# Optimization experiments

Measured on AMD Instinct MI355X. Metric: run time of the kernel, lower is better.

## Reference

```python
import jax, jax.numpy as jnp
import numpy as np

N = 50000       # nodes
E = 800000      # edges (before self-loops)
F_IN = 128      # per-head input features (nfeat * t_size, t_size=1)
NHID = 128
NHEADS = 4
NCLASS = 64
NEG_SLOPE = 0.2   # GATConv leakyrelu negative_slope
ALPHA = 0.2       # outer LeakyReLU(alpha)


def setup_inputs():
    key = jax.random.key(0)
    ks = jax.random.split(key, 10)
    type_emb = jax.random.normal(ks[0], (NHEADS, N, F_IN), jnp.float32)
    edge = jax.random.randint(ks[1], (2, E), 0, N, dtype=jnp.int32)
    W = jax.random.normal(ks[2], (NHEADS, F_IN, NHID), jnp.float32) / np.sqrt(F_IN).astype(np.float32)
    att_src = jax.random.normal(ks[3], (NHEADS, NHID), jnp.float32) * 0.1
    att_dst = jax.random.normal(ks[4], (NHEADS, NHID), jnp.float32) * 0.1
    bias = jnp.zeros((NHEADS, NHID), jnp.float32)
    W_out = jax.random.normal(ks[5], (NHID * NHEADS, NCLASS), jnp.float32) / np.sqrt(NHID * NHEADS).astype(np.float32)
    att_src_out = jax.random.normal(ks[6], (NCLASS,), jnp.float32) * 0.1
    att_dst_out = jax.random.normal(ks[7], (NCLASS,), jnp.float32) * 0.1
    bias_out = jnp.zeros((NCLASS,), jnp.float32)
    return {"type_emb": type_emb, "edge": edge, "W": W, "att_src": att_src,
            "att_dst": att_dst, "bias": bias, "W_out": W_out,
            "att_src_out": att_src_out, "att_dst_out": att_dst_out,
            "bias_out": bias_out}


def _gat_conv(x, src, dst, W, a_src, a_dst, b):
    """PyG GATConv, heads=1, with self-loops already in (src, dst)."""
    xs = x @ W                                      # [N, H]
    e = jax.nn.leaky_relu((xs @ a_src)[src] + (xs @ a_dst)[dst], NEG_SLOPE)  # [E']
    # segment softmax over destination nodes (every node has a self-loop -> no empty segment)
    m = jax.ops.segment_max(e, dst, num_segments=N)
    ex = jnp.exp(e - m[dst])
    denom = jax.ops.segment_sum(ex, dst, num_segments=N)
    alpha = ex / denom[dst]                          # [E']
    out = jax.ops.segment_sum(alpha[:, None] * xs[src], dst, num_segments=N)  # [N, H]
    return out + b


def reference(type_emb, edge, W, att_src, att_dst, bias, W_out,
              att_src_out, att_dst_out, bias_out):
    loop = jnp.arange(N, dtype=edge.dtype)
    src = jnp.concatenate([edge[0], loop])
    dst = jnp.concatenate([edge[1], loop])
    # per-head GraphAttentionLayer: GATConv -> LeakyReLU(alpha) (dropout inactive)
    heads = [jax.nn.leaky_relu(
                 _gat_conv(type_emb[i], src, dst, W[i], att_src[i], att_dst[i], bias[i]),
                 ALPHA)
             for i in range(NHEADS)]
    x = jnp.concatenate(heads, axis=1)               # [N, NHID*NHEADS]
    y = jax.nn.leaky_relu(
            _gat_conv(x, src, dst, W_out, att_src_out, att_dst_out, bias_out),
            ALPHA)
    return jnp.tanh(y)                               # [N, NCLASS]
```

## Files before the change

kernel.cpp:

```cpp
#include <hip/hip_runtime.h>
#include <cmath>

#define NN 50000
#define EE 800000
#define ETOT (EE + NN)
#define NSCAN ((NN + 1023) / 1024)
#define SROWS 50048

typedef __bf16 v8bf __attribute__((ext_vector_type(8)));
typedef float f32x4 __attribute__((ext_vector_type(4)));
typedef float f32x2 __attribute__((ext_vector_type(2)));

__device__ __forceinline__ float lrelu(float x){ return x > 0.0f ? x : 0.2f * x; }
__device__ __forceinline__ unsigned short f2bf_rne(float x){
  unsigned int u = __float_as_uint(x);
  u += 0x7fffu + ((u >> 16) & 1u);
  return (unsigned short)(u >> 16);
}
__device__ __forceinline__ float bf2f(unsigned short b){
  return __uint_as_float(((unsigned int)b) << 16);
}
__device__ __forceinline__ void fma8p(f32x2* acc, float w, uint4 u){
  f32x2 w2 = {w, w};
  f32x2 a0, a1, a2, a3;
  a0[0] = __uint_as_float(u.x << 16); a0[1] = __uint_as_float(u.x & 0xffff0000u);
  a1[0] = __uint_as_float(u.y << 16); a1[1] = __uint_as_float(u.y & 0xffff0000u);
  a2[0] = __uint_as_float(u.z << 16); a2[1] = __uint_as_float(u.z & 0xffff0000u);
  a3[0] = __uint_as_float(u.w << 16); a3[1] = __uint_as_float(u.w & 0xffff0000u);
  acc[0] += w2 * a0;
  acc[1] += w2 * a1;
  acc[2] += w2 * a2;
  acc[3] += w2 * a3;
}

__global__ void k_hist(const int* __restrict__ dst, int* __restrict__ cnt){
  int i = blockIdx.x * 256 + threadIdx.x;
  if (i >= ETOT) return;
  int d = (i < EE) ? dst[i] : (i - EE);
  atomicAdd(&cnt[d], 1);
}

__global__ void k_scan1(const int* __restrict__ cnt, int* __restrict__ part){
  __shared__ int sm[256];
  int b = blockIdx.x, t = threadIdx.x;
  int base = b * 1024 + t * 4;
  int s = 0;
  #pragma unroll
  for (int j = 0; j < 4; j++) if (base + j < NN) s += cnt[base + j];
  sm[t] = s; __syncthreads();
  for (int off = 128; off; off >>= 1){
    if (t < off) sm[t] += sm[t + off];
    __syncthreads();
  }
  if (t == 0) part[b] = sm[0];
}

__global__ void k_scan2(const int* __restrict__ part, int* __restrict__ part2){
  if (threadIdx.x == 0 && blockIdx.x == 0){
    int run = 0;
    for (int i = 0; i < NSCAN; i++){ part2[i] = run; run += part[i]; }
  }
}

__global__ void k_scan3(const int* __restrict__ cnt, const int* __restrict__ part2,
                        int* __restrict__ rowptr){
  __shared__ int sm[256];
  int b = blockIdx.x, t = threadIdx.x;
  int base = b * 1024 + t * 4;
  int v[4]; int s = 0;
  #pragma unroll
  for (int j = 0; j < 4; j++){ v[j] = (base + j < NN) ? cnt[base + j] : 0; s += v[j]; }
  sm[t] = s; __syncthreads();
  for (int off = 1; off < 256; off <<= 1){
    int x = (t >= off) ? sm[t - off] : 0;
    __syncthreads();
    sm[t] += x;
    __syncthreads();
  }
  int run = part2[b] + sm[t] - s;
  #pragma unroll
  for (int j = 0; j < 4; j++){
    if (base + j < NN){ rowptr[base + j] = run; run += v[j]; }
  }
  if (b == 0 && t == 0) rowptr[NN] = ETOT;
}

__global__ void k_scatter(const int* __restrict__ src, const int* __restrict__ dst,
                          const int* __restrict__ rowptr, int* __restrict__ fill,
                          int* __restrict__ csr){
  int i = blockIdx.x * 256 + threadIdx.x;
  if (i >= ETOT) return;
  int s, d;
  if (i < EE){ s = src[i]; d = dst[i]; } else { s = d = i - EE; }
  int pos = rowptr[d] + atomicAdd(&fill[d], 1);
  csr[pos] = s;
}

__global__ void k_convB(const float* __restrict__ B, unsigned short* __restrict__ bh,
                        unsigned short* __restrict__ bl, int K, int N, int total){
  int i = blockIdx.x * 256 + threadIdx.x;
  if (i >= total) return;
  int per = K * N;
  int h = i / per, rem = i - h * per;
  int k = rem / N, n = rem - k * N;
  float x = B[i];
  unsigned short hb = f2bf_rne(x);
  unsigned short lb = f2bf_rne(x - bf2f(hb));
  size_t o = (size_t)h * per + ((size_t)(k >> 3) * N + n) * 8 + (k & 7);
  bh[o] = hb; bl[o] = lb;
}

template<int BN, int OSTR>
__global__ __launch_bounds__(256) void gemm_split(const float* __restrict__ A,
                                                  const unsigned short* __restrict__ Bh,
                                                  const unsigned short* __restrict__ Bl,
                                                  unsigned short* __restrict__ out,
                                                  int M, int K,
                                                  const float* __restrict__ att_s,
                                                  const float* __restrict__ att_d,
                                                  float* __restrict__ ssrc,
                                                  float* __restrict__ sdst){
  const int t = threadIdx.x;
  const int wv = t >> 6, lane = t & 63;
  const int m0 = blockIdx.x * 128;
  const int h = blockIdx.y;
  A  += (size_t)h * M * K;
  Bh += (size_t)h * (K >> 3) * BN * 8;
  Bl += (size_t)h * (K >> 3) * BN * 8;
  const int colOff = h * BN;

  __shared__ v8bf sAh[4][128];
  __shared__ v8bf sAl[4][128];
  __shared__ v8bf sBh[4][BN];
  __shared__ v8bf sBl[4][BN];

  f32x4 acc[2][BN / 16];
  #pragma unroll
  for (int i = 0; i < 2; i++)
    #pragma unroll
    for (int j = 0; j < BN / 16; j++){
      f32x4 z = {0.f, 0.f, 0.f, 0.f};
      acc[i][j] = z;
    }

  const int mRow = t & 127;
  const int kh = (t >> 7) * 16;
  const bool valid = (m0 + mRow) < M;
  const int q = lane >> 4, lm = lane & 15;

  for (int k0 = 0; k0 < K; k0 += 32){
    const float* ap = A + (size_t)(m0 + mRow) * K + k0 + kh;
    float4 v0, v1, v2, v3;
    if (valid){
      v0 = *(const float4*)(ap);
      v1 = *(const float4*)(ap + 4);
      v2 = *(const float4*)(ap + 8);
      v3 = *(const float4*)(ap + 12);
    } else {
      v0 = v1 = v2 = v3 = make_float4(0.f, 0.f, 0.f, 0.f);
    }
    #pragma unroll
    for (int g = 0; g < 2; g++){
      float xv[8];
      if (g == 0){ xv[0]=v0.x; xv[1]=v0.y; xv[2]=v0.z; xv[3]=v0.w; xv[4]=v1.x; xv[5]=v1.y; xv[6]=v1.z; xv[7]=v1.w; }
      else       { xv[0]=v2.x; xv[1]=v2.y; xv[2]=v2.z; xv[3]=v2.w; xv[4]=v3.x; xv[5]=v3.y; xv[6]=v3.z; xv[7]=v3.w; }
      v8bf H, L;
      #pragma unroll
      for (int i = 0; i < 8; i++){
        __bf16 hb = (__bf16)xv[i];
        float  hf = (float)hb;
        H[i] = hb;
        L[i] = (__bf16)(xv[i] - hf);
      }
      int k8 = (kh >> 3) + g;
      sAh[k8][mRow] = H;
      sAl[k8][mRow] = L;
    }
    {
      const v8bf* gh = (const v8bf*)Bh + (size_t)(k0 >> 3) * BN;
      const v8bf* gl = (const v8bf*)Bl + (size_t)(k0 >> 3) * BN;
      v8bf* dh = &sBh[0][0];
      v8bf* dl = &sBl[0][0];
      #pragma unroll
      for (int i = t; i < 4 * BN; i += 256){ dh[i] = gh[i]; dl[i] = gl[i]; }
    }
    __syncthreads();
    v8bf ah[2], al[2];
    #pragma unroll
    for (int rt = 0; rt < 2; rt++){
      int m = wv * 32 + rt * 16 + lm;
      ah[rt] = sAh[q][m];
      al[rt] = sAl[q][m];
    }
    #pragma unroll
    for (int ct = 0; ct < BN / 16; ct++){
      v8bf bh = sBh[q][ct * 16 + lm];
      v8bf bl = sBl[q][ct * 16 + lm];
      #pragma unroll
      for (int rt = 0; rt < 2; rt++){
        acc[rt][ct] = __builtin_amdgcn_mfma_f32_16x16x32_bf16(ah[rt], bh, acc[rt][ct], 0, 0, 0);
        acc[rt][ct] = __builtin_amdgcn_mfma_f32_16x16x32_bf16(ah[rt], bl, acc[rt][ct], 0, 0, 0);
        acc[rt][ct] = __builtin_amdgcn_mfma_f32_16x16x32_bf16(al[rt], bh, acc[rt][ct], 0, 0, 0);
      }
    }
    __syncthreads();
  }

  float asv[BN / 16], adv[BN / 16];
  #pragma unroll
  for (int ct = 0; ct < BN / 16; ct++){
    asv[ct] = att_s[h * BN + ct * 16 + lm];
    adv[ct] = att_d[h * BN + ct * 16 + lm];
  }

  #pragma unroll
  for (int rt = 0; rt < 2; rt++){
    #pragma unroll
    for (int reg = 0; reg < 4; reg++){
      int r = m0 + wv * 32 + rt * 16 + q * 4 + reg;
      float d0 = 0.f, d1 = 0.f;
      #pragma unroll
      for (int ct = 0; ct < BN / 16; ct++){
        float v = acc[rt][ct][reg];
        d0 += v * asv[ct];
        d1 += v * adv[ct];
      }
      #pragma unroll
      for (int off = 1; off < 16; off <<= 1){
        d0 += __shfl_xor(d0, off, 64);
        d1 += __shfl_xor(d1, off, 64);
      }
      if (r < M){
        unsigned short* orow = out + (size_t)r * OSTR + colOff + lm;
        #pragma unroll
        for (int ct = 0; ct < BN / 16; ct++)
          orow[ct * 16] = f2bf_rne(acc[rt][ct][reg]);
        if (lm == 0){
          ssrc[(size_t)h * SROWS + r] = d0;
          sdst[(size_t)h * SROWS + r] = d1;
        }
      }
    }
  }
}

template<int BN, int OSTR>
__global__ __launch_bounds__(256) void gemm_ps(const unsigned short* __restrict__ Ah,
                                               const unsigned short* __restrict__ Bh,
                                               const unsigned short* __restrict__ Bl,
                                               unsigned short* __restrict__ out,
                                               int M, int K,
                                               const float* __restrict__ att_s,
                                               const float* __restrict__ att_d,
                                               float* __restrict__ ssrc,
                                               float* __restrict__ sdst){
  const int t = threadIdx.x;
  const int wv = t >> 6, lane = t & 63;
  const int m0 = blockIdx.x * 128;
  const int h = blockIdx.y;
  const int colOff = h * BN;

  __shared__ v8bf sAh[4][128];
  __shared__ v8bf sBh[4][BN];
  __shared__ v8bf sBl[4][BN];

  f32x4 acc[2][BN / 16];
  #pragma unroll
  for (int i = 0; i < 2; i++)
    #pragma unroll
    for (int j = 0; j < BN / 16; j++){
      f32x4 z = {0.f, 0.f, 0.f, 0.f};
      acc[i][j] = z;
    }

  const int mRow = t & 127;
  const int kh = (t >> 7) * 16;
  const bool valid = (m0 + mRow) < M;
  const int q = lane >> 4, lm = lane & 15;

  for (int k0 = 0; k0 < K; k0 += 32){
    const unsigned short* aph = Ah + (size_t)(m0 + mRow) * K + k0 + kh;
    uint4 h0, h1;
    if (valid){
      h0 = *(const uint4*)(aph);
      h1 = *(const uint4*)(aph + 8);
    } else {
      h0 = h1 = make_uint4(0, 0, 0, 0);
    }
    int k8 = kh >> 3;
    sAh[k8][mRow]     = *(v8bf*)&h0;
    sAh[k8 + 1][mRow] = *(v8bf*)&h1;
    {
      const v8bf* gh = (const v8bf*)Bh + (size_t)(k0 >> 3) * BN;
      const v8bf* gl = (const v8bf*)Bl + (size_t)(k0 >> 3) * BN;
      v8bf* dh = &sBh[0][0];
      v8bf* dl = &sBl[0][0];
      #pragma unroll
      for (int i = t; i < 4 * BN; i += 256){ dh[i] = gh[i]; dl[i] = gl[i]; }
    }
    __syncthreads();
    v8bf ah[2];
    #pragma unroll
    for (int rt = 0; rt < 2; rt++){
      int m = wv * 32 + rt * 16 + lm;
      ah[rt] = sAh[q][m];
    }
    #pragma unroll
    for (int ct = 0; ct < BN / 16; ct++){
      v8bf bh = sBh[q][ct * 16 + lm];
      v8bf bl = sBl[q][ct * 16 + lm];
      #pragma unroll
      for (int rt = 0; rt < 2; rt++){
        acc[rt][ct] = __builtin_amdgcn_mfma_f32_16x16x32_bf16(ah[rt], bh, acc[rt][ct], 0, 0, 0);
        acc[rt][ct] = __builtin_amdgcn_mfma_f32_16x16x32_bf16(ah[rt], bl, acc[rt][ct], 0, 0, 0);
      }
    }
    __syncthreads();
  }

  float asv[BN / 16], adv[BN / 16];
  #pragma unroll
  for (int ct = 0; ct < BN / 16; ct++){
    asv[ct] = att_s[h * BN + ct * 16 + lm];
    adv[ct] = att_d[h * BN + ct * 16 + lm];
  }

  #pragma unroll
  for (int rt = 0; rt < 2; rt++){
    #pragma unroll
    for (int reg = 0; reg < 4; reg++){
      int r = m0 + wv * 32 + rt * 16 + q * 4 + reg;
      float d0 = 0.f, d1 = 0.f;
      #pragma unroll
      for (int ct = 0; ct < BN / 16; ct++){
        float v = acc[rt][ct][reg];
        d0 += v * asv[ct];
        d1 += v * adv[ct];
      }
      #pragma unroll
      for (int off = 1; off < 16; off <<= 1){
        d0 += __shfl_xor(d0, off, 64);
        d1 += __shfl_xor(d1, off, 64);
      }
      if (r < M){
        unsigned short* orow = out + (size_t)r * OSTR + colOff + lm;
        #pragma unroll
        for (int ct = 0; ct < BN / 16; ct++)
          orow[ct * 16] = f2bf_rne(acc[rt][ct][reg]);
        if (lm == 0){
          ssrc[(size_t)h * SROWS + r] = d0;
          sdst[(size_t)h * SROWS + r] = d1;
        }
      }
    }
  }
}

__global__ __launch_bounds__(256) void k_agg1(const int* __restrict__ rowptr,
                                              const int* __restrict__ csr,
                                              const float* __restrict__ ssrc,
                                              const float* __restrict__ sdst,
                                              const unsigned short* __restrict__ xs_all,
                                              const float* __restrict__ bias,
                                              unsigned short* __restrict__ x1h){
  int tid = blockIdx.x * 256 + threadIdx.x;
  int n = tid >> 4;
  int lm = threadIdx.x & 15;
  int h = blockIdx.y;
  if (n >= NN) return;
  int start = rowptr[n], end = rowptr[n + 1];
  const float* sp = ssrc + (size_t)h * SROWS;
  float sdn = sdst[(size_t)h * SROWS + n];
  const uint4* xp = (const uint4*)xs_all + h * 16 + lm;

  float sloc = 0.f;
  f32x2 acc[4];
  #pragma unroll
  for (int i = 0; i < 4; i++){ f32x2 z = {0.f, 0.f}; acc[i] = z; }

  int e = start;
  int sA = csr[e];
  float svA = sp[sA];
  uint4 uA = xp[(size_t)sA * 64];
  for (; e + 1 < end; e++){
    int sB = csr[e + 1];
    float svB = sp[sB];
    uint4 uB = xp[(size_t)sB * 64];
    float w = __expf(lrelu(svA + sdn));
    sloc += w;
    fma8p(acc, w, uA);
    svA = svB; uA = uB;
  }
  float w = __expf(lrelu(svA + sdn));
  sloc += w;
  fma8p(acc, w, uA);

  float inv = 1.f / sloc;

  const float* bp = bias + h * 128 + lm * 8;
  float4 b0 = *(const float4*)bp, b1 = *(const float4*)(bp + 4);
  float bb[8] = {b0.x, b0.y, b0.z, b0.w, b1.x, b1.y, b1.z, b1.w};
  union { uint4 q; unsigned short u[8]; } HH;
  #pragma unroll
  for (int i = 0; i < 8; i++){
    float o = lrelu(acc[i >> 1][i & 1] * inv + bb[i]);
    HH.u[i] = f2bf_rne(o);
  }
  size_t ofs = (size_t)n * 512 + h * 128 + lm * 8;
  *(uint4*)(x1h + ofs) = HH.q;
}

__global__ __launch_bounds__(256) void k_agg2(const int* __restrict__ rowptr,
                                              const int* __restrict__ csr,
                                              const float* __restrict__ ssrc,
                                              const float* __restrict__ sdst,
                                              const unsigned short* __restrict__ xs2,
                                              const float* __restrict__ bias,
                                              float* __restrict__ outp){
  int tid = blockIdx.x * 256 + threadIdx.x;
  int n = tid >> 3;
  int lm = threadIdx.x & 7;
  if (n >= NN) return;
  int start = rowptr[n], end = rowptr[n + 1];
  float sdn = sdst[n];
  const uint4* xp = (const uint4*)xs2 + lm;

  float sloc = 0.f;
  f32x2 acc[4];
  #pragma unroll
  for (int i = 0; i < 4; i++){ f32x2 z = {0.f, 0.f}; acc[i] = z; }

  int e = start;
  int sA = csr[e];
  float svA = ssrc[sA];
  uint4 uA = xp[(size_t)sA * 8];
  for (; e + 1 < end; e++){
    int sB = csr[e + 1];
    float svB = ssrc[sB];
    uint4 uB = xp[(size_t)sB * 8];
    float w = __expf(lrelu(svA + sdn));
    sloc += w;
    fma8p(acc, w, uA);
    svA = svB; uA = uB;
  }
  float w = __expf(lrelu(svA + sdn));
  sloc += w;
  fma8p(acc, w, uA);

  float inv = 1.f / sloc;

  float o[8];
  #pragma unroll
  for (int i = 0; i < 8; i++)
    o[i] = tanhf(lrelu(acc[i >> 1][i & 1] * inv + bias[lm * 8 + i]));
  float* op = outp + (size_t)n * 64 + lm * 8;
  *(float4*)op       = make_float4(o[0], o[1], o[2], o[3]);
  *(float4*)(op + 4) = make_float4(o[4], o[5], o[6], o[7]);
}

extern "C" void kernel_launch(void* const* d_in, const int* in_sizes, int n_in,
                              void* d_out, int out_size, void* d_ws, size_t ws_size,
                              hipStream_t stream){
  const float* type_emb  = (const float*)d_in[0];
  const int*   edge      = (const int*)d_in[1];
  const float* W         = (const float*)d_in[2];
  const float* att_src   = (const float*)d_in[3];
  const float* att_dst   = (const float*)d_in[4];
  const float* bias      = (const float*)d_in[5];
  const float* W_out     = (const float*)d_in[6];
  const float* att_src_o = (const float*)d_in[7];
  const float* att_dst_o = (const float*)d_in[8];
  const float* bias_o    = (const float*)d_in[9];
  float* out = (float*)d_out;
  (void)in_sizes; (void)n_in; (void)out_size; (void)ws_size;

  char* ws = (char*)d_ws;
  size_t off = 0;
  auto alloc = [&](size_t bytes) -> void* {
    void* p = ws + off;
    off = (off + bytes + 255) & ~(size_t)255;
    return p;
  };
  unsigned short* xs_all = (unsigned short*)alloc((size_t)NN * 512 * 2);
  unsigned short* x1h    = (unsigned short*)alloc((size_t)NN * 512 * 2);
  unsigned short* xs2    = (unsigned short*)alloc((size_t)NN * 64 * 2);
  float* ssrc1 = (float*)alloc((size_t)4 * SROWS * 4);
  float* sdst1 = (float*)alloc((size_t)4 * SROWS * 4);
  float* ssrc2 = (float*)alloc((size_t)SROWS * 4);
  float* sdst2 = (float*)alloc((size_t)SROWS * 4);
  int* cnt    = (int*)alloc((size_t)NN * 4);
  int* rowptr = (int*)alloc((size_t)(NN + 1) * 4);
  int* fill   = (int*)alloc((size_t)NN * 4);
  int* csr    = (int*)alloc((size_t)ETOT * 4);
  int* p1     = (int*)alloc((size_t)NSCAN * 4 + 256);
  int* p2     = (int*)alloc((size_t)NSCAN * 4 + 256);
  unsigned short* Bh1 = (unsigned short*)alloc((size_t)4 * 128 * 128 * 2);
  unsigned short* Bl1 = (unsigned short*)alloc((size_t)4 * 128 * 128 * 2);
  unsigned short* Bh2 = (unsigned short*)alloc((size_t)512 * 64 * 2);
  unsigned short* Bl2 = (unsigned short*)alloc((size_t)512 * 64 * 2);

  hipMemsetAsync(cnt, 0, (size_t)NN * 4, stream);
  hipMemsetAsync(fill, 0, (size_t)NN * 4, stream);
  k_hist<<<(ETOT + 255) / 256, 256, 0, stream>>>(edge + EE, cnt);
  k_scan1<<<NSCAN, 256, 0, stream>>>(cnt, p1);
  k_scan2<<<1, 64, 0, stream>>>(p1, p2);
  k_scan3<<<NSCAN, 256, 0, stream>>>(cnt, p2, rowptr);
  k_scatter<<<(ETOT + 255) / 256, 256, 0, stream>>>(edge, edge + EE, rowptr, fill, csr);

  k_convB<<<(4 * 128 * 128 + 255) / 256, 256, 0, stream>>>(W, Bh1, Bl1, 128, 128, 4 * 128 * 128);
  k_convB<<<(512 * 64 + 255) / 256, 256, 0, stream>>>(W_out, Bh2, Bl2, 512, 64, 512 * 64);

  gemm_split<128, 512><<<dim3(391, 4), 256, 0, stream>>>(
      type_emb, Bh1, Bl1, xs_all, NN, 128, att_src, att_dst, ssrc1, sdst1);
  k_agg1<<<dim3(3125, 4), 256, 0, stream>>>(rowptr, csr, ssrc1, sdst1, xs_all, bias, x1h);

  gemm_ps<64, 64><<<dim3(391, 1), 256, 0, stream>>>(
      x1h, Bh2, Bl2, xs2, NN, 512, att_src_o, att_dst_o, ssrc2, sdst2);
  k_agg2<<<1563, 256, 0, stream>>>(rowptr, csr, ssrc2, sdst2, xs2, bias_o, out);
}
```

Before: 441.5 us.

## Fold attention vectors into padded weight columns and drop A low-part split

Precomputes W·att_src and W·att_dst as two extra weight columns, padding the first-layer B matrix to 144 columns, so the GEMM produces the attention scores directly instead of doing an epilogue dot product and shuffle reduction. It also drops the bf16 low-part of the A operand, cutting one of three MFMAs per tile and the A low shared buffer. The extra columns add a wider tile and more accumulator registers. Dropping the A residual lowers input precision to roughly bf16 for type_emb, which may affect accuracy.

After: 456.3 us. 3.4% more time.

```diff
diff --git a/kernel.cpp b/kernel.cpp
--- a/kernel.cpp
+++ b/kernel.cpp
@@ -97,7 +97,7 @@
 }
 
 __global__ void k_convB(const float* __restrict__ B, unsigned short* __restrict__ bh,
-                        unsigned short* __restrict__ bl, int K, int N, int total){
+                        unsigned short* __restrict__ bl, int K, int N, int NX, int total){
   int i = blockIdx.x * 256 + threadIdx.x;
   if (i >= total) return;
   int per = K * N;
@@ -106,18 +106,35 @@
   float x = B[i];
   unsigned short hb = f2bf_rne(x);
   unsigned short lb = f2bf_rne(x - bf2f(hb));
-  size_t o = (size_t)h * per + ((size_t)(k >> 3) * N + n) * 8 + (k & 7);
+  size_t o = (size_t)h * (K >> 3) * NX * 8 + ((size_t)(k >> 3) * NX + n) * 8 + (k & 7);
   bh[o] = hb; bl[o] = lb;
 }
 
-template<int BN, int OSTR>
+__global__ void k_convAtt(const float* __restrict__ W, const float* __restrict__ att_s,
+                          const float* __restrict__ att_d,
+                          unsigned short* __restrict__ bh, unsigned short* __restrict__ bl,
+                          int K, int N, int NX){
+  int h = blockIdx.x, k = threadIdx.x;
+  const float* wrow = W + ((size_t)h * K + k) * N;
+  const float* as = att_s + (size_t)h * N;
+  const float* ad = att_d + (size_t)h * N;
+  float s = 0.f, d = 0.f;
+  for (int n = 0; n < N; n++){ float w = wrow[n]; s += w * as[n]; d += w * ad[n]; }
+  size_t base = (size_t)h * (K >> 3) * NX * 8 + (size_t)(k >> 3) * NX * 8 + (k & 7);
+  unsigned short hs = f2bf_rne(s);
+  bh[base + (size_t)N * 8] = hs;
+  bl[base + (size_t)N * 8] = f2bf_rne(s - bf2f(hs));
+  unsigned short hd = f2bf_rne(d);
+  bh[base + (size_t)(N + 1) * 8] = hd;
+  bl[base + (size_t)(N + 1) * 8] = f2bf_rne(d - bf2f(hd));
+}
+
+template<int BN, int BNX, int OSTR>
 __global__ __launch_bounds__(256) void gemm_split(const float* __restrict__ A,
                                                   const unsigned short* __restrict__ Bh,
                                                   const unsigned short* __restrict__ Bl,
                                                   unsigned short* __restrict__ out,
                                                   int M, int K,
-                                                  const float* __restrict__ att_s,
-                                                  const float* __restrict__ att_d,
                                                   float* __restrict__ ssrc,
                                                   float* __restrict__ sdst){
   const int t = threadIdx.x;
@@ -125,20 +142,19 @@
   const int m0 = blockIdx.x * 128;
   const int h = blockIdx.y;
   A  += (size_t)h * M * K;
-  Bh += (size_t)h * (K >> 3) * BN * 8;
-  Bl += (size_t)h * (K >> 3) * BN * 8;
+  Bh += (size_t)h * (K >> 3) * BNX * 8;
+  Bl += (size_t)h * (K >> 3) * BNX * 8;
   const int colOff = h * BN;
 
-  __shared__ v8bf sAh[4][128];
-  __shared__ v8bf sAl[4][128];
-  __shared__ v8bf sBh[4][BN];
-  __shared__ v8bf sBl[4][BN];
-
-  f32x4 acc[2][BN / 16];
+  __shared__ v8bf sA[4][128];
+  __shared__ v8bf sBh[4][BNX];
+  __shared__ v8bf sBl[4][BNX];
+
+  f32x4 acc[2][BNX / 16];
   #pragma unroll
   for (int i = 0; i < 2; i++)
     #pragma unroll
-    for (int j = 0; j < BN / 16; j++){
+    for (int j = 0; j < BNX / 16; j++){
       f32x4 z = {0.f, 0.f, 0.f, 0.f};
       acc[i][j] = z;
     }
@@ -164,53 +180,35 @@
       float xv[8];
       if (g == 0){ xv[0]=v0.x; xv[1]=v0.y; xv[2]=v0.z; xv[3]=v0.w; xv[4]=v1.x; xv[5]=v1.y; xv[6]=v1.z; xv[7]=v1.w; }
       else       { xv[0]=v2.x; xv[1]=v2.y; xv[2]=v2.z; xv[3]=v2.w; xv[4]=v3.x; xv[5]=v3.y; xv[6]=v3.z; xv[7]=v3.w; }
-      v8bf H, L;
-      #pragma unroll
-      for (int i = 0; i < 8; i++){
-        __bf16 hb = (__bf16)xv[i];
-        float  hf = (float)hb;
-        H[i] = hb;
-        L[i] = (__bf16)(xv[i] - hf);
-      }
-      int k8 = (kh >> 3) + g;
-      sAh[k8][mRow] = H;
-      sAl[k8][mRow] = L;
+      v8bf H;
+      #pragma unroll
+      for (int i = 0; i < 8; i++) H[i] = (__bf16)xv[i];
+      sA[(kh >> 3) + g][mRow] = H;
     }
     {
-      const v8bf* gh = (const v8bf*)Bh + (size_t)(k0 >> 3) * BN;
-      const v8bf* gl = (const v8bf*)Bl + (size_t)(k0 >> 3) * BN;
+      const v8bf* gh = (const v8bf*)Bh + (size_t)(k0 >> 3) * BNX;
+      const v8bf* gl = (const v8bf*)Bl + (size_t)(k0 >> 3) * BNX;
       v8bf* dh = &sBh[0][0];
       v8bf* dl = &sBl[0][0];
       #pragma unroll
-      for (int i = t; i < 4 * BN; i += 256){ dh[i] = gh[i]; dl[i] = gl[i]; }
-    }
-    __syncthreads();
-    v8bf ah[2], al[2];
-    #pragma unroll
-    for (int rt = 0; rt < 2; rt++){
-      int m = wv * 32 + rt * 16 + lm;
-      ah[rt] = sAh[q][m];
-      al[rt] = sAl[q][m];
-    }
-    #pragma unroll
-    for (int ct = 0; ct < BN / 16; ct++){
+      for (int i = t; i < 4 * BNX; i += 256){ dh[i] = gh[i]; dl[i] = gl[i]; }
+    }
+    __syncthreads();
+    v8bf ah[2];
+    #pragma unroll
+    for (int rt = 0; rt < 2; rt++)
+      ah[rt] = sA[q][wv * 32 + rt * 16 + lm];
+    #pragma unroll
+    for (int ct = 0; ct < BNX / 16; ct++){
       v8bf bh = sBh[q][ct * 16 + lm];
       v8bf bl = sBl[q][ct * 16 + lm];
       #pragma unroll
       for (int rt = 0; rt < 2; rt++){
         acc[rt][ct] = __builtin_amdgcn_mfma_f32_16x16x32_bf16(ah[rt], bh, acc[rt][ct], 0, 0, 0);
         acc[rt][ct] = __builtin_amdgcn_mfma_f32_16x16x32_bf16(ah[rt], bl, acc[rt][ct], 0, 0, 0);
-        acc[rt][ct] = __builtin_amdgcn_mfma_f32_16x16x32_bf16(al[rt], bh, acc[rt][ct], 0, 0, 0);
       }
     }
     __syncthreads();
-  }
-
-  float asv[BN / 16], adv[BN / 16];
-  #pragma unroll
-  for (int ct = 0; ct < BN / 16; ct++){
-    asv[ct] = att_s[h * BN + ct * 16 + lm];
-    adv[ct] = att_d[h * BN + ct * 16 + lm];
   }
 
   #pragma unroll
@@ -218,27 +216,14 @@
     #pragma unroll
     for (int reg = 0; reg < 4; reg++){
       int r = m0 + wv * 32 + rt * 16 + q * 4 + reg;
-      float d0 = 0.f, d1 = 0.f;
-      #pragma unroll
-      for (int ct = 0; ct < BN / 16; ct++){
-        float v = acc[rt][ct][reg];
-        d0 += v * asv[ct];
-        d1 += v * adv[ct];
-      }
-      #pragma unroll
-      for (int off = 1; off < 16; off <<= 1){
-        d0 += __shfl_xor(d0, off, 64);
-        d1 += __shfl_xor(d1, off, 64);
-      }
       if (r < M){
         unsigned short* orow = out + (size_t)r * OSTR + colOff + lm;
         #pragma unroll
         for (int ct = 0; ct < BN / 16; ct++)
           orow[ct * 16] = f2bf_rne(acc[rt][ct][reg]);
-        if (lm == 0){
-          ssrc[(size_t)h * SROWS + r] = d0;
-          sdst[(size_t)h * SROWS + r] = d1;
-        }
+        float v = acc[rt][BN / 16][reg];
+        if (lm == 0) ssrc[(size_t)h * SROWS + r] = v;
+        else if (lm == 1) sdst[(size_t)h * SROWS + r] = v;
       }
     }
   }
@@ -494,24 +479,28 @@
   int* csr    = (int*)alloc((size_t)ETOT * 4);
   int* p1     = (int*)alloc((size_t)NSCAN * 4 + 256);
   int* p2     = (int*)alloc((size_t)NSCAN * 4 + 256);
-  unsigned short* Bh1 = (unsigned short*)alloc((size_t)4 * 128 * 128 * 2);
-  unsigned short* Bl1 = (unsigned short*)alloc((size_t)4 * 128 * 128 * 2);
+  size_t b1elems = (size_t)4 * 16 * 144 * 8;
+  unsigned short* Bh1 = (unsigned short*)alloc(b1elems * 2);
+  unsigned short* Bl1 = (unsigned short*)alloc(b1elems * 2);
   unsigned short* Bh2 = (unsigned short*)alloc((size_t)512 * 64 * 2);
   unsigned short* Bl2 = (unsigned short*)alloc((size_t)512 * 64 * 2);
 
   hipMemsetAsync(cnt, 0, (size_t)NN * 4, stream);
   hipMemsetAsync(fill, 0, (size_t)NN * 4, stream);
+  hipMemsetAsync(Bh1, 0, b1elems * 2, stream);
+  hipMemsetAsync(Bl1, 0, b1elems * 2, stream);
   k_hist<<<(ETOT + 255) / 256, 256, 0, stream>>>(edge + EE, cnt);
   k_scan1<<<NSCAN, 256, 0, stream>>>(cnt, p1);
   k_scan2<<<1, 64, 0, stream>>>(p1, p2);
   k_scan3<<<NSCAN, 256, 0, stream>>>(cnt, p2, rowptr);
   k_scatter<<<(ETOT + 255) / 256, 256, 0, stream>>>(edge, edge + EE, rowptr, fill, csr);
 
-  k_convB<<<(4 * 128 * 128 + 255) / 256, 256, 0, stream>>>(W, Bh1, Bl1, 128, 128, 4 * 128 * 128);
-  k_convB<<<(512 * 64 + 255) / 256, 256, 0, stream>>>(W_out, Bh2, Bl2, 512, 64, 512 * 64);
-
-  gemm_split<128, 512><<<dim3(391, 4), 256, 0, stream>>>(
-      type_emb, Bh1, Bl1, xs_all, NN, 128, att_src, att_dst, ssrc1, sdst1);
+  k_convB<<<(4 * 128 * 128 + 255) / 256, 256, 0, stream>>>(W, Bh1, Bl1, 128, 128, 144, 4 * 128 * 128);
+  k_convAtt<<<4, 128, 0, stream>>>(W, att_src, att_dst, Bh1, Bl1, 128, 128, 144);
+  k_convB<<<(512 * 64 + 255) / 256, 256, 0, stream>>>(W_out, Bh2, Bl2, 512, 64, 64, 512 * 64);
+
+  gemm_split<128, 144, 512><<<dim3(391, 4), 256, 0, stream>>>(
+      type_emb, Bh1, Bl1, xs_all, NN, 128, ssrc1, sdst1);
   k_agg1<<<dim3(3125, 4), 256, 0, stream>>>(rowptr, csr, ssrc1, sdst1, xs_all, bias, x1h);
 
   gemm_ps<64, 64><<<dim3(391, 1), 256, 0, stream>>>(
```
